# Optimization experiments

Measured on AMD Instinct MI355X. Metric: run time of the kernel, lower is better.

The kernel has to match this reference:

```python
import jax, jax.numpy as jnp
import numpy as np

DIM = 1024
B, N = 8, 4096
EPS = 1e-6


def setup_inputs() -> dict:
    key = jax.random.key(0)
    k1, k2, k3, k4 = jax.random.split(key, 4)
    x = jax.random.normal(k1, (B, N, DIM), dtype=jnp.float32)
    # torch nn.Linear weights: W_qkv [3*dim, dim], W_out [dim, dim], b_out [dim]
    s = 1.0 / np.sqrt(DIM)
    W_qkv = jax.random.uniform(k2, (3 * DIM, DIM), jnp.float32, -s, s)
    W_out = jax.random.uniform(k3, (DIM, DIM), jnp.float32, -s, s)
    b_out = jax.random.uniform(k4, (DIM,), jnp.float32, -s, s)
    return {"x": x, "W_qkv": W_qkv, "W_out": W_out, "b_out": b_out}


def reference(x, W_qkv, W_out, b_out):
    # qkv projection (Linear without bias): x @ W_qkv.T -> [B,N,3D]
    qkv = jnp.einsum('bnd,ed->bne', x, W_qkv)
    q, k, v = jnp.split(qkv, 3, axis=-1)
    q = jax.nn.relu(q) + EPS
    k = jax.nn.relu(k) + EPS
    # kv accumulation: [B,D,D]
    kv = jnp.einsum('bnd,bne->bde', k, v)
    # normalizer z: [B,N]
    z = 1.0 / (jnp.einsum('bnd,bd->bn', q, k.sum(axis=1)) + EPS)
    # attn output: [B,N,D]
    attn = jnp.einsum('bnd,bde,bn->bne', q, kv, z)
    # output projection with bias
    return jnp.einsum('bne,fe->bnf', attn, W_out) + b_out
```

## Files before the change

kernel.cpp:

```cpp
#include <hip/hip_runtime.h>


#define EPS 1e-6f

using u16 = unsigned short;
typedef __attribute__((ext_vector_type(4))) float f32x4;
typedef __attribute__((ext_vector_type(8))) __bf16 bf16x8;

__device__ __forceinline__ u16 f2b(float f) {
  unsigned u = __builtin_bit_cast(unsigned, f);
  u += 0x7FFFu + ((u >> 16) & 1u);
  return (u16)(u >> 16);
}
__device__ __forceinline__ float b2f(u16 h) {
  return __builtin_bit_cast(float, (unsigned)h << 16);
}

typedef const __attribute__((address_space(1))) void* gas1_t;
typedef __attribute__((address_space(3))) void* las3_t;

__device__ __forceinline__ void load16_to_lds(const void* g, void* l) {
  __builtin_amdgcn_global_load_lds((gas1_t)g, (las3_t)l, 16, 0, 0);
}

#define BARRIER() do { asm volatile("" ::: "memory"); __builtin_amdgcn_s_barrier(); asm volatile("" ::: "memory"); } while (0)
#define WAITL0()  do { asm volatile("s_waitcnt lgkmcnt(0)" ::: "memory"); __builtin_amdgcn_sched_barrier(0); } while (0)
#define WAITV(n)  asm volatile("s_waitcnt vmcnt(" #n ")" ::: "memory")
#define MFMA16(a, b, c) __builtin_amdgcn_mfma_f32_16x16x32_bf16((a), (b), (c), 0, 0, 0)

__device__ __forceinline__ void stage_half(const u16* g, int ld, u16* l,
                                           int r0, int csw, int woff) {
  load16_to_lds(g + (long long)r0 * ld + csw, l + woff);
  load16_to_lds(g + (long long)(r0 + 64) * ld + csw, l + 4096 + woff);
}

template<int MODE>
__global__ __launch_bounds__(512, 2) void gemm256(
    const u16* __restrict__ A, const u16* __restrict__ B, void* __restrict__ Cv,
    int M, int N, int K, int lda, int ldb, int ldc,
    long long sA, long long sB, long long sC,
    const float* __restrict__ zvec, const float* __restrict__ bias,
    u16* __restrict__ kT, u16* __restrict__ vT, float* __restrict__ ksum)
{
  __shared__ __align__(16) u16 shA[32768];
  __shared__ __align__(16) u16 shB[32768];

  const int tid  = threadIdx.x;
  const int lane = tid & 63, wave = tid >> 6;
  const int wr = wave >> 2, wc = wave & 3;
  const int quad = lane >> 4, lc = lane & 15;

  const int TN = gridDim.y;
  const int lin = blockIdx.x + gridDim.x * blockIdx.y;
  const int xcd = lin & 7, g = lin >> 3;
  const int bm = (g / TN) * 8 + xcd;
  const int bn = g % TN;
  const int bz = blockIdx.z;
  const u16* Ab = A + (long long)bz * sA;
  const u16* Bb = B + (long long)bz * sB;

  const int r0   = tid >> 3;
  const int csw  = (((tid & 7) ^ ((tid >> 3) & 7)) << 3);
  const int woff = wave * 512;

  const int ch0 = ((quad ^ (lane & 7)) << 3);
  const int ch1 = (((4 + quad) ^ (lane & 7)) << 3);
  const int aRow = wr * 128 + lc;
  const int bRow = wc * 64 + lc;

  const int NT = K >> 6;

  f32x4 acc[8][4];
  #pragma unroll
  for (int i = 0; i < 8; ++i)
    #pragma unroll
    for (int j = 0; j < 4; ++j) acc[i][j] = f32x4{0.f, 0.f, 0.f, 0.f};

  auto stA = [&](int h, int t) {
    stage_half(Ab + ((long long)bm * 256 + h * 128) * lda + t * 64, lda,
               shA + (t & 1) * 16384 + h * 8192, r0, csw, woff);
  };
  auto stB = [&](int h, int t) {
    stage_half(Bb + ((long long)bn * 256 + h * 128) * ldb + t * 64, ldb,
               shB + (t & 1) * 16384 + h * 8192, r0, csw, woff);
  };

  bf16x8 aF[4][2], aG[4][2], b01[2][2], b23[2][2];

  stA(0, 0); stA(1, 0); stB(0, 0); stB(1, 0);
  if (NT > 1) { stB(0, 1); stA(0, 1); stA(1, 1); WAITV(6); }
  else        { WAITV(0); }
  BARRIER();
  #pragma unroll
  for (int i = 0; i < 4; ++i) {
    aF[i][0] = *(const bf16x8*)&shA[(aRow + i * 16) * 64 + ch0];
    aF[i][1] = *(const bf16x8*)&shA[(aRow + i * 16) * 64 + ch1];
  }

  for (int t = 0; t < NT; ++t) {
    const u16* aB = shA + (t & 1) * 16384;
    const u16* bB = shB + (t & 1) * 16384;
    const u16* aN = shA + ((t + 1) & 1) * 16384;

    #pragma unroll
    for (int j = 0; j < 2; ++j) {
      b01[j][0] = *(const bf16x8*)&bB[(bRow + j * 16) * 64 + ch0];
      b01[j][1] = *(const bf16x8*)&bB[(bRow + j * 16) * 64 + ch1];
    }
    if (t + 1 < NT) stB(1, t + 1);
    BARRIER(); WAITL0();
    __builtin_amdgcn_s_setprio(1);
    #pragma unroll
    for (int i = 0; i < 4; ++i)
      #pragma unroll
      for (int j = 0; j < 2; ++j) {
        acc[i][j] = MFMA16(aF[i][0], b01[j][0], acc[i][j]);
        acc[i][j] = MFMA16(aF[i][1], b01[j][1], acc[i][j]);
      }
    __builtin_amdgcn_s_setprio(0);
    BARRIER();

    #pragma unroll
    for (int j = 0; j < 2; ++j) {
      b23[j][0] = *(const bf16x8*)&bB[(bRow + (2 + j) * 16) * 64 + ch0];
      b23[j][1] = *(const bf16x8*)&bB[(bRow + (2 + j) * 16) * 64 + ch1];
    }
    BARRIER(); WAITL0();
    __builtin_amdgcn_s_setprio(1);
    #pragma unroll
    for (int i = 0; i < 4; ++i)
      #pragma unroll
      for (int j = 0; j < 2; ++j) {
        acc[i][2 + j] = MFMA16(aF[i][0], b23[j][0], acc[i][2 + j]);
        acc[i][2 + j] = MFMA16(aF[i][1], b23[j][1], acc[i][2 + j]);
      }
    __builtin_amdgcn_s_setprio(0);
    BARRIER();

    #pragma unroll
    for (int i = 0; i < 4; ++i) {
      aG[i][0] = *(const bf16x8*)&aB[(aRow + (4 + i) * 16) * 64 + ch0];
      aG[i][1] = *(const bf16x8*)&aB[(aRow + (4 + i) * 16) * 64 + ch1];
    }
    if (t + 2 < NT) stB(0, t + 2);
    BARRIER(); WAITL0();
    __builtin_amdgcn_s_setprio(1);
    #pragma unroll
    for (int i = 0; i < 4; ++i)
      #pragma unroll
      for (int j = 0; j < 2; ++j) {
        acc[4 + i][j] = MFMA16(aG[i][0], b01[j][0], acc[4 + i][j]);
        acc[4 + i][j] = MFMA16(aG[i][1], b01[j][1], acc[4 + i][j]);
      }
    __builtin_amdgcn_s_setprio(0);
    if (t + 2 < NT) { WAITV(2); } else { WAITV(0); }
    BARRIER();

    if (t + 1 < NT) {
      #pragma unroll
      for (int i = 0; i < 4; ++i) {
        aF[i][0] = *(const bf16x8*)&aN[(aRow + i * 16) * 64 + ch0];
        aF[i][1] = *(const bf16x8*)&aN[(aRow + i * 16) * 64 + ch1];
      }
    }
    if (t + 2 < NT) { stA(0, t + 2); stA(1, t + 2); }
    BARRIER();
    __builtin_amdgcn_s_setprio(1);
    #pragma unroll
    for (int i = 0; i < 4; ++i)
      #pragma unroll
      for (int j = 0; j < 2; ++j) {
        acc[4 + i][2 + j] = MFMA16(aG[i][0], b23[j][0], acc[4 + i][2 + j]);
        acc[4 + i][2 + j] = MFMA16(aG[i][1], b23[j][1], acc[4 + i][2 + j]);
      }
    __builtin_amdgcn_s_setprio(0);
    BARRIER();
  }

  const long long rowb = (long long)bm * 256 + wr * 128 + quad * 4;
  const int colb = bn * 256 + wc * 64 + lc;

  if (MODE == 0) {
    const int region = colb >> 10;
    if (region == 0) {
      u16* q = (u16*)Cv;
      #pragma unroll
      for (int i = 0; i < 8; ++i)
        #pragma unroll
        for (int j = 0; j < 4; ++j) {
          const int col = colb + j * 16;
          #pragma unroll
          for (int r = 0; r < 4; ++r) {
            const long long row = rowb + i * 16 + r;
            q[row * ldc + col] = f2b(fmaxf(acc[i][j][r], 0.f) + EPS);
          }
        }
    } else {
      const bool isk = (region == 1);
      const int b = (int)(rowb >> 12);
      u16* dst = (isk ? kT : vT) + (long long)b * 1024 * 4096;
      const int nloc = (int)(rowb & 4095);
      #pragma unroll
      for (int j = 0; j < 4; ++j) {
        const int d = colb + j * 16 - region * 1024;
        float s = 0.f;
        #pragma unroll
        for (int i = 0; i < 8; ++i) {
          ushort4 pk;
          #pragma unroll
          for (int r = 0; r < 4; ++r) {
            float v = acc[i][j][r];
            if (isk) { v = fmaxf(v, 0.f) + EPS; s += v; }
            (&pk.x)[r] = f2b(v);
          }
          *(ushort4*)(dst + (long long)d * 4096 + nloc + i * 16) = pk;
        }
        if (isk) {
          s += __shfl_xor(s, 16);
          s += __shfl_xor(s, 32);
          if (quad == 0) atomicAdd(&ksum[b * 1024 + d], s);
        }
      }
    }
  } else if (MODE == 2) {
    float* out = (float*)Cv + (long long)bz * sC;
    #pragma unroll
    for (int i = 0; i < 8; ++i)
      #pragma unroll
      for (int j = 0; j < 4; ++j) {
        const int col = colb + j * 16;
        const float bj = bias[col];
        #pragma unroll
        for (int r = 0; r < 4; ++r) {
          const long long row = rowb + i * 16 + r;
          out[row * ldc + col] = acc[i][j][r] * zvec[(long long)bz * M + row] + bj;
        }
      }
  } else {
    u16* out = (u16*)Cv + (long long)bz * sC;
    #pragma unroll
    for (int i = 0; i < 8; ++i)
      #pragma unroll
      for (int j = 0; j < 4; ++j) {
        const int col = colb + j * 16;
        #pragma unroll
        for (int r = 0; r < 4; ++r) {
          const long long row = rowb + i * 16 + r;
          out[row * ldc + col] = f2b(acc[i][j][r]);
        }
      }
  }
}

template<int MODE>
__global__ __launch_bounds__(256) void gemm_abT(
    const u16* __restrict__ A, const u16* __restrict__ B, void* __restrict__ Cv,
    int M, int N, int K, int lda, int ldb, int ldc,
    long long sA, long long sB, long long sC,
    const float* __restrict__ zvec, const float* __restrict__ bias,
    u16* __restrict__ kT, u16* __restrict__ vT, float* __restrict__ ksum)
{
  __shared__ u16 lA[128 * 32];
  __shared__ u16 lB[128 * 32];
  const int tid  = threadIdx.x;
  const int wave = tid >> 6, lane = tid & 63;
  const int TN = gridDim.y;
  const int lin = blockIdx.x + gridDim.x * blockIdx.y;
  const int xcd = lin & 7, g = lin >> 3;
  const int bm = (g / TN) * 8 + xcd;
  const int bn = g % TN;
  const int bz = blockIdx.z;
  const u16* Ab = A + (long long)bz * sA;
  const u16* Bb = B + (long long)bz * sB;

  const int c0 = wave * 64 + lane;
  const int c1 = 256 + c0;
  const u16* gA0 = Ab + (long long)(bm * 128 + (c0 >> 2)) * lda + (c0 & 3) * 8;
  const u16* gA1 = Ab + (long long)(bm * 128 + (c1 >> 2)) * lda + (c1 & 3) * 8;
  const u16* gB0 = Bb + (long long)(bn * 128 + (c0 >> 2)) * ldb + (c0 & 3) * 8;
  const u16* gB1 = Bb + (long long)(bn * 128 + (c1 >> 2)) * ldb + (c1 & 3) * 8;
  u16* lA0 = &lA[(wave * 64) * 8];
  u16* lA1 = &lA[(256 + wave * 64) * 8];
  u16* lB0 = &lB[(wave * 64) * 8];
  u16* lB1 = &lB[(256 + wave * 64) * 8];

  const int wm = (wave & 1) * 64, wn = (wave >> 1) * 64;
  const int aoff = (wm + (lane & 15)) * 32 + (lane >> 4) * 8;
  const int boff = (wn + (lane & 15)) * 32 + (lane >> 4) * 8;

  f32x4 acc[4][4];
  #pragma unroll
  for (int i = 0; i < 4; i++)
    #pragma unroll
    for (int j = 0; j < 4; j++) acc[i][j] = f32x4{0.f, 0.f, 0.f, 0.f};

  for (int k0 = 0; k0 < K; k0 += 32) {
    load16_to_lds(gA0 + k0, lA0);
    load16_to_lds(gA1 + k0, lA1);
    load16_to_lds(gB0 + k0, lB0);
    load16_to_lds(gB1 + k0, lB1);
    __syncthreads();
    bf16x8 af[4], bfv[4];
    #pragma unroll
    for (int i = 0; i < 4; i++) af[i]  = *(const bf16x8*)&lA[aoff + i * 16 * 32];
    #pragma unroll
    for (int j = 0; j < 4; j++) bfv[j] = *(const bf16x8*)&lB[boff + j * 16 * 32];
    #pragma unroll
    for (int i = 0; i < 4; i++)
      #pragma unroll
      for (int j = 0; j < 4; j++)
        acc[i][j] = MFMA16(af[i], bfv[j], acc[i][j]);
    __syncthreads();
  }

  const int quad = lane >> 4, lc = lane & 15;
  const int rowb = bm * 128 + wm + quad * 4;
  const int colb = bn * 128 + wn + lc;

  #pragma unroll
  for (int i = 0; i < 4; i++) {
    #pragma unroll
    for (int j = 0; j < 4; j++) {
      const int col = colb + j * 16;
      float bj = 0.f;
      if (MODE == 2) bj = bias[col];
      #pragma unroll
      for (int r = 0; r < 4; r++) {
        const int row = rowb + i * 16 + r;
        float v = acc[i][j][r];
        if (MODE == 1) {
          ((u16*)Cv + (long long)bz * sC)[(long long)row * ldc + col] = f2b(v);
        } else if (MODE == 2) {
          float zz = zvec[(long long)bz * M + row];
          ((float*)Cv + (long long)bz * sC)[(long long)row * ldc + col] = v * zz + bj;
        }
      }
    }
  }
  (void)kT; (void)vT; (void)ksum;
}

__global__ void cvt_f32_bf16(const float* __restrict__ s, u16* __restrict__ d, int n4) {
  int i = blockIdx.x * blockDim.x + threadIdx.x;
  int st = gridDim.x * blockDim.x;
  for (; i < n4; i += st) {
    float4 f = ((const float4*)s)[i];
    uint2 o;
    o.x = (unsigned)f2b(f.x) | ((unsigned)f2b(f.y) << 16);
    o.y = (unsigned)f2b(f.z) | ((unsigned)f2b(f.w) << 16);
    ((uint2*)d)[i] = o;
  }
}

__global__ void zero_f32(float* __restrict__ p, int n) {
  int i = blockIdx.x * blockDim.x + threadIdx.x;
  if (i < n) p[i] = 0.f;
}

__global__ void z_kernel(const u16* __restrict__ qbuf, const float* __restrict__ ksum,
                         float* __restrict__ z) {
  const int row  = blockIdx.x * 4 + (threadIdx.x >> 6);
  const int lane = threadIdx.x & 63;
  const int b = row >> 12;
  const uint4* q = (const uint4*)(qbuf + (long long)row * 1024);
  const float* ks = ksum + b * 1024;
  float s = 0.f;
  #pragma unroll
  for (int c = 0; c < 2; c++) {
    int idx = lane + c * 64;
    uint4 d = q[idx];
    unsigned w[4] = {d.x, d.y, d.z, d.w};
    const float* kk = ks + idx * 8;
    #pragma unroll
    for (int qq = 0; qq < 4; qq++)
      s += b2f((u16)(w[qq] & 0xFFFF)) * kk[qq * 2]
         + b2f((u16)(w[qq] >> 16))    * kk[qq * 2 + 1];
  }
  #pragma unroll
  for (int o = 32; o > 0; o >>= 1) s += __shfl_down(s, o);
  if (lane == 0) z[row] = 1.0f / (s + EPS);
}

extern "C" void kernel_launch(void* const* d_in, const int* in_sizes, int n_in,
                              void* d_out, int out_size, void* d_ws, size_t ws_size,
                              hipStream_t stream) {
  const float* x    = (const float*)d_in[0];
  const float* Wqkv = (const float*)d_in[1];
  const float* Wout = (const float*)d_in[2];
  const float* bout = (const float*)d_in[3];

  char* ws = (char*)d_ws;
  u16* x_bf    = (u16*)(ws + 0);
  u16* qbuf    = (u16*)(ws + 67108864);
  u16* kT      = (u16*)(ws + 134217728);
  u16* vT      = (u16*)(ws + 201326592);
  u16* wqkv_bf = (u16*)(ws + 268435456);
  u16* wout_bf = (u16*)(ws + 274726912);
  u16* kv      = (u16*)(ws + 276824064);
  u16* kvwT    = (u16*)(ws + 293601280);
  float* ksum  = (float*)(ws + 310378496);
  float* z     = (float*)(ws + 310411264);

  cvt_f32_bf16<<<4096, 256, 0, stream>>>(x,    x_bf,    33554432 / 4);
  cvt_f32_bf16<<<1024, 256, 0, stream>>>(Wqkv, wqkv_bf,  3145728 / 4);
  cvt_f32_bf16<<<512,  256, 0, stream>>>(Wout, wout_bf,  1048576 / 4);
  zero_f32<<<32, 256, 0, stream>>>(ksum, 8192);

  gemm256<0><<<dim3(128, 12, 1), 512, 0, stream>>>(
      x_bf, wqkv_bf, qbuf, 32768, 3072, 1024, 1024, 1024, 1024,
      0, 0, 0, nullptr, nullptr, kT, vT, ksum);

  z_kernel<<<8192, 256, 0, stream>>>(qbuf, ksum, z);

  gemm_abT<1><<<dim3(8, 8, 8), 256, 0, stream>>>(
      kT, vT, kv, 1024, 1024, 4096, 4096, 4096, 1024,
      4194304, 4194304, 1048576, nullptr, nullptr, nullptr, nullptr, nullptr);

  gemm_abT<1><<<dim3(8, 8, 8), 256, 0, stream>>>(
      wout_bf, kv, kvwT, 1024, 1024, 1024, 1024, 1024, 1024,
      0, 1048576, 1048576, nullptr, nullptr, nullptr, nullptr, nullptr);

  gemm256<2><<<dim3(16, 4, 8), 512, 0, stream>>>(
      qbuf, kvwT, d_out, 4096, 1024, 1024, 1024, 1024, 1024,
      4194304, 1048576, 4194304, z, bout, nullptr, nullptr, nullptr);
}
```

Measured before the change: 711.5 us.

## Reschedule GEMM main loop to prefetch LDS fragments one phase ahead

Reorders the four MFMA phases of the 256x256 GEMM loop so that each phase's LDS fragment reads (b23, aG, next aF, next b01) are issued one phase before they are consumed. The explicit lgkmcnt(0) waits are dropped in favour of sched barriers plus the compiler's own waits. The global-to-LDS staging for tile t+2 is now issued all at once after a full vmcnt(0) drain in mid-iteration, replacing the staggered per-half staging. The aim is to hide LDS read latency behind MFMA work. The cost is more live registers and a coarser global-load overlap window.

```diff
diff --git a/kernel.cpp b/kernel.cpp
--- a/kernel.cpp
+++ b/kernel.cpp
@@ -24,7 +24,7 @@
 }
 
 #define BARRIER() do { asm volatile("" ::: "memory"); __builtin_amdgcn_s_barrier(); asm volatile("" ::: "memory"); } while (0)
-#define WAITL0()  do { asm volatile("s_waitcnt lgkmcnt(0)" ::: "memory"); __builtin_amdgcn_sched_barrier(0); } while (0)
+#define SCHED0()  __builtin_amdgcn_sched_barrier(0)
 #define WAITV(n)  asm volatile("s_waitcnt vmcnt(" #n ")" ::: "memory")
 #define MFMA16(a, b, c) __builtin_amdgcn_mfma_f32_16x16x32_bf16((a), (b), (c), 0, 0, 0)
 
@@ -84,31 +84,38 @@
     stage_half(Bb + ((long long)bn * 256 + h * 128) * ldb + t * 64, ldb,
                shB + (t & 1) * 16384 + h * 8192, r0, csw, woff);
   };
+  auto stAll = [&](int t) { stA(0, t); stA(1, t); stB(0, t); stB(1, t); };
 
   bf16x8 aF[4][2], aG[4][2], b01[2][2], b23[2][2];
 
-  stA(0, 0); stA(1, 0); stB(0, 0); stB(1, 0);
-  if (NT > 1) { stB(0, 1); stA(0, 1); stA(1, 1); WAITV(6); }
+  stAll(0);
+  if (NT > 1) { stAll(1); WAITV(8); }
   else        { WAITV(0); }
   BARRIER();
   #pragma unroll
   for (int i = 0; i < 4; ++i) {
     aF[i][0] = *(const bf16x8*)&shA[(aRow + i * 16) * 64 + ch0];
     aF[i][1] = *(const bf16x8*)&shA[(aRow + i * 16) * 64 + ch1];
+  }
+  #pragma unroll
+  for (int j = 0; j < 2; ++j) {
+    b01[j][0] = *(const bf16x8*)&shB[(bRow + j * 16) * 64 + ch0];
+    b01[j][1] = *(const bf16x8*)&shB[(bRow + j * 16) * 64 + ch1];
   }
 
   for (int t = 0; t < NT; ++t) {
     const u16* aB = shA + (t & 1) * 16384;
     const u16* bB = shB + (t & 1) * 16384;
     const u16* aN = shA + ((t + 1) & 1) * 16384;
+    const u16* bN = shB + ((t + 1) & 1) * 16384;
+    const bool rdn = (t + 1 < NT);
 
     #pragma unroll
     for (int j = 0; j < 2; ++j) {
-      b01[j][0] = *(const bf16x8*)&bB[(bRow + j * 16) * 64 + ch0];
-      b01[j][1] = *(const bf16x8*)&bB[(bRow + j * 16) * 64 + ch1];
-    }
-    if (t + 1 < NT) stB(1, t + 1);
-    BARRIER(); WAITL0();
+      b23[j][0] = *(const bf16x8*)&bB[(bRow + (2 + j) * 16) * 64 + ch0];
+      b23[j][1] = *(const bf16x8*)&bB[(bRow + (2 + j) * 16) * 64 + ch1];
+    }
+    BARRIER(); SCHED0();
     __builtin_amdgcn_s_setprio(1);
     #pragma unroll
     for (int i = 0; i < 4; ++i)
@@ -118,14 +125,14 @@
         acc[i][j] = MFMA16(aF[i][1], b01[j][1], acc[i][j]);
       }
     __builtin_amdgcn_s_setprio(0);
-    BARRIER();
-
-    #pragma unroll
-    for (int j = 0; j < 2; ++j) {
-      b23[j][0] = *(const bf16x8*)&bB[(bRow + (2 + j) * 16) * 64 + ch0];
-      b23[j][1] = *(const bf16x8*)&bB[(bRow + (2 + j) * 16) * 64 + ch1];
-    }
-    BARRIER(); WAITL0();
+    SCHED0(); BARRIER();
+
+    #pragma unroll
+    for (int i = 0; i < 4; ++i) {
+      aG[i][0] = *(const bf16x8*)&aB[(aRow + (4 + i) * 16) * 64 + ch0];
+      aG[i][1] = *(const bf16x8*)&aB[(aRow + (4 + i) * 16) * 64 + ch1];
+    }
+    BARRIER(); SCHED0();
     __builtin_amdgcn_s_setprio(1);
     #pragma unroll
     for (int i = 0; i < 4; ++i)
@@ -135,15 +142,18 @@
         acc[i][2 + j] = MFMA16(aF[i][1], b23[j][1], acc[i][2 + j]);
       }
     __builtin_amdgcn_s_setprio(0);
+    SCHED0();
+    WAITV(0);
     BARRIER();
 
-    #pragma unroll
-    for (int i = 0; i < 4; ++i) {
-      aG[i][0] = *(const bf16x8*)&aB[(aRow + (4 + i) * 16) * 64 + ch0];
-      aG[i][1] = *(const bf16x8*)&aB[(aRow + (4 + i) * 16) * 64 + ch1];
-    }
-    if (t + 2 < NT) stB(0, t + 2);
-    BARRIER(); WAITL0();
+    if (rdn) {
+      #pragma unroll
+      for (int i = 0; i < 4; ++i) {
+        aF[i][0] = *(const bf16x8*)&aN[(aRow + i * 16) * 64 + ch0];
+        aF[i][1] = *(const bf16x8*)&aN[(aRow + i * 16) * 64 + ch1];
+      }
+    }
+    BARRIER(); SCHED0();
     __builtin_amdgcn_s_setprio(1);
     #pragma unroll
     for (int i = 0; i < 4; ++i)
@@ -153,18 +163,17 @@
         acc[4 + i][j] = MFMA16(aG[i][1], b01[j][1], acc[4 + i][j]);
       }
     __builtin_amdgcn_s_setprio(0);
-    if (t + 2 < NT) { WAITV(2); } else { WAITV(0); }
-    BARRIER();
-
-    if (t + 1 < NT) {
-      #pragma unroll
-      for (int i = 0; i < 4; ++i) {
-        aF[i][0] = *(const bf16x8*)&aN[(aRow + i * 16) * 64 + ch0];
-        aF[i][1] = *(const bf16x8*)&aN[(aRow + i * 16) * 64 + ch1];
-      }
-    }
-    if (t + 2 < NT) { stA(0, t + 2); stA(1, t + 2); }
-    BARRIER();
+    SCHED0(); BARRIER();
+
+    if (t + 2 < NT) stAll(t + 2);
+    if (rdn) {
+      #pragma unroll
+      for (int j = 0; j < 2; ++j) {
+        b01[j][0] = *(const bf16x8*)&bN[(bRow + j * 16) * 64 + ch0];
+        b01[j][1] = *(const bf16x8*)&bN[(bRow + j * 16) * 64 + ch1];
+      }
+    }
+    BARRIER(); SCHED0();
     __builtin_amdgcn_s_setprio(1);
     #pragma unroll
     for (int i = 0; i < 4; ++i)
@@ -174,7 +183,7 @@
         acc[4 + i][2 + j] = MFMA16(aG[i][1], b23[j][1], acc[4 + i][2 + j]);
       }
     __builtin_amdgcn_s_setprio(0);
-    BARRIER();
+    SCHED0(); BARRIER();
   }
 
   const long long rowb = (long long)bm * 256 + wr * 128 + quad * 4;
```

Result: slower. 766.0 us (+7.7%).
